# Performance work log

Measured on AMD Instinct MI355X. Metric: run time of the kernel, lower is better.

Reference implementation:

```python
import jax, jax.numpy as jnp
import numpy as np
from jax.scipy.special import logsumexp

B, T = 32, 512
WV, CV = 32000, 8000
DW, DC = 128, 64
H = 128          # hidden per direction (hidden_size // 2)
L = 32           # num_labels


def setup_inputs() -> dict:
    key = jax.random.key(0)
    ks = jax.random.split(key, 16)
    D = DW + DC
    def n(k, shape, s=0.1):
        return jax.random.normal(k, shape, jnp.float32) * s
    return {
        'word': jax.random.randint(ks[0], (B, T), 1, WV),
        'char': jax.random.randint(ks[1], (B, T), 1, CV),  # >0 so mask is all ones
        'y': jax.random.randint(ks[2], (B, T), 0, L),
        'wordemb': n(ks[3], (WV, DW)),
        'charemb': n(ks[4], (CV, DC)),
        'W_ih_f': n(ks[5], (4 * H, D)), 'W_hh_f': n(ks[6], (4 * H, H)), 'b_f': n(ks[7], (4 * H,)),
        'W_ih_b': n(ks[8], (4 * H, D)), 'W_hh_b': n(ks[9], (4 * H, H)), 'b_b': n(ks[10], (4 * H,)),
        'W_out': n(ks[11], (L, 2 * H)), 'b_out': n(ks[12], (L,)),
        'trans': n(ks[13], (L, L)), 'start': n(ks[14], (L,)), 'end': n(ks[15], (L,)),
    }


def _lstm_scan(x_proj, W_hh):
    # x_proj: [T, B, 4H] = x @ W_ih.T + b, precomputed (batched GEMM)
    h0 = jnp.zeros((x_proj.shape[1], W_hh.shape[1]), x_proj.dtype)
    def step(carry, xt):
        h, c = carry
        g = xt + h @ W_hh.T                      # [B, 4H]
        i, f, gg, o = jnp.split(g, 4, axis=-1)   # PyTorch gate order i,f,g,o
        c = jax.nn.sigmoid(f) * c + jax.nn.sigmoid(i) * jnp.tanh(gg)
        h = jax.nn.sigmoid(o) * jnp.tanh(c)
        return (h, c), h
    _, hs = jax.lax.scan(step, (h0, h0), x_proj)
    return hs  # [T, B, H]


def reference(word, char, y, wordemb, charemb, W_ih_f, W_hh_f, b_f,
              W_ih_b, W_hh_b, b_b, W_out, b_out, trans, start, end):
    mask = (char > 0).astype(jnp.float32)                 # [B, T]
    x = jnp.concatenate([wordemb[word], charemb[char]], axis=-1)  # [B, T, D]

    # BiLSTM
    xp_f = (jnp.einsum('btd,gd->tbg', x, W_ih_f) + b_f)   # [T, B, 4H]
    xp_b = (jnp.einsum('btd,gd->tbg', x, W_ih_b) + b_b)[::-1]
    h_f = _lstm_scan(xp_f, W_hh_f)                        # [T, B, H]
    h_b = _lstm_scan(xp_b, W_hh_b)[::-1]                  # [T, B, H]
    h = jnp.concatenate([h_f, h_b], axis=-1).transpose(1, 0, 2)  # [B, T, 2H]

    emit = (jnp.einsum('bth,lh->btl', h, W_out) + b_out) * mask[:, :, None]  # [B, T, L]

    # CRF log-partition (forward algorithm)
    alpha0 = start + emit[:, 0]                           # [B, L]
    def crf_step(alpha, inp):
        e_t, m_t = inp                                    # [B, L], [B]
        new = logsumexp(alpha[:, :, None] + trans, axis=1) + e_t
        alpha = jnp.where(m_t[:, None] > 0, new, alpha)
        return alpha, None
    alpha, _ = jax.lax.scan(crf_step, alpha0,
                            (emit.transpose(1, 0, 2)[1:], mask.T[1:]))
    logZ = logsumexp(alpha + end, axis=-1)                # [B]

    # gold path score
    emit_score = (jnp.take_along_axis(emit, y[:, :, None], axis=-1)[..., 0] * mask).sum(1)
    trans_score = (trans[y[:, :-1], y[:, 1:]] * mask[:, 1:]).sum(1)
    last = mask.sum(1).astype(jnp.int32) - 1
    y_last = y[jnp.arange(y.shape[0]), last]
    gold = start[y[:, 0]] + emit_score + trans_score + end[y_last]

    return jnp.sum(logZ - gold)  # NLL, summed over batch
```

## Files before the change

kernel.cpp:

```cpp
#include <hip/hip_runtime.h>
#include <math.h>

#define BB 32
#define TT 512
#define DW 128
#define DC 64
#define DD 192
#define HH 128
#define G4 512
#define LL 32

typedef __fp16 h2_t __attribute__((ext_vector_type(2)));

__device__ __forceinline__ float qxor1(float x) {
    return __int_as_float(__builtin_amdgcn_update_dpp(0, __float_as_int(x), 0xB1, 0xF, 0xF, true));
}
__device__ __forceinline__ float qxor2(float x) {
    return __int_as_float(__builtin_amdgcn_update_dpp(0, __float_as_int(x), 0x4E, 0xF, 0xF, true));
}
__device__ __forceinline__ float qbcast(float x, int ctrl_imm) {
    switch (ctrl_imm) {
        case 0: return __int_as_float(__builtin_amdgcn_update_dpp(0, __float_as_int(x), 0x00, 0xF, 0xF, true));
        case 1: return __int_as_float(__builtin_amdgcn_update_dpp(0, __float_as_int(x), 0x55, 0xF, 0xF, true));
        case 2: return __int_as_float(__builtin_amdgcn_update_dpp(0, __float_as_int(x), 0xAA, 0xF, 0xF, true));
        default:return __int_as_float(__builtin_amdgcn_update_dpp(0, __float_as_int(x), 0xFF, 0xF, 0xF, true));
    }
}

__global__ __launch_bounds__(256) void k_inproj(
    const int* __restrict__ word, const int* __restrict__ charr,
    const float* __restrict__ wemb, const float* __restrict__ cemb,
    const float* __restrict__ Wf, const float* __restrict__ bf,
    const float* __restrict__ Wb, const float* __restrict__ bb,
    float* __restrict__ xpf, float* __restrict__ xpb)
{
    __shared__ __align__(16) h2_t As2[4][132];
    __shared__ __align__(16) h2_t Bs2[4][132];
    const int tid = threadIdx.x;
    const int ntile = blockIdx.x;
    const int ctile = blockIdx.y;
    const int dir = ctile >> 2;
    const float* W = dir ? Wb : Wf;
    const float* bias = dir ? bb : bf;
    float* xp = dir ? xpb : xpf;
    const int colbase = (ctile & 3) * 128;

    const int tr = tid >> 4;
    const int tc = tid & 15;

    float acc[8][8];
#pragma unroll
    for (int i = 0; i < 8; ++i)
#pragma unroll
        for (int j = 0; j < 8; ++j) acc[i][j] = 0.f;

    const int lrow = tid >> 1;
    const int lk   = (tid & 1) * 4;
    const int kp0  = lk >> 1;
    const int nA   = ntile * 128 + lrow;
    const int wi   = word[nA];
    const int ci   = charr[nA];
    const int g    = colbase + lrow;

    for (int kc = 0; kc < 24; ++kc) {
        const int k0 = kc * 8 + lk;
        float4 av;
        if (k0 < DW) av = *(const float4*)(wemb + (size_t)wi * DW + k0);
        else         av = *(const float4*)(cemb + (size_t)ci * DC + (k0 - DW));
        const float4 bv = *(const float4*)(W + (size_t)g * DD + k0);
        __syncthreads();
        As2[kp0 + 0][lrow] = __builtin_amdgcn_cvt_pkrtz(av.x, av.y);
        As2[kp0 + 1][lrow] = __builtin_amdgcn_cvt_pkrtz(av.z, av.w);
        Bs2[kp0 + 0][lrow] = __builtin_amdgcn_cvt_pkrtz(bv.x, bv.y);
        Bs2[kp0 + 1][lrow] = __builtin_amdgcn_cvt_pkrtz(bv.z, bv.w);
        __syncthreads();
#pragma unroll
        for (int kp = 0; kp < 4; ++kp) {
            h2_t __attribute__((aligned(16))) a2[8], b2[8];
            *(uint4*)&a2[0] = *(const uint4*)&As2[kp][tr * 8];
            *(uint4*)&a2[4] = *(const uint4*)&As2[kp][tr * 8 + 4];
            *(uint4*)&b2[0] = *(const uint4*)&Bs2[kp][tc * 8];
            *(uint4*)&b2[4] = *(const uint4*)&Bs2[kp][tc * 8 + 4];
#pragma unroll
            for (int i = 0; i < 8; ++i)
#pragma unroll
                for (int j = 0; j < 8; ++j)
                    acc[i][j] = __builtin_amdgcn_fdot2(a2[i], b2[j], acc[i][j], false);
        }
    }
#pragma unroll
    for (int i = 0; i < 8; ++i) {
        const int n  = ntile * 128 + tr * 8 + i;
        const int b_ = n >> 9, t_ = n & 511;
        float* dst = xp + ((size_t)(t_ * BB + b_)) * G4 + colbase + tc * 8;
#pragma unroll
        for (int j = 0; j < 8; ++j) dst[j] = acc[i][j] + bias[colbase + tc * 8 + j];
    }
}

__global__ __launch_bounds__(512)
__attribute__((amdgpu_waves_per_eu(2, 2)))
void k_lstm(
    const float* __restrict__ xpf, const float* __restrict__ xpb,
    const float* __restrict__ Whf, const float* __restrict__ Whb,
    float* __restrict__ hf, float* __restrict__ hb)
{
    __shared__ __align__(16) __fp16 hsd[2][160];
    const int tid = threadIdx.x;
    const int dir = blockIdx.x >> 5;
    const int b_  = blockIdx.x & 31;
    const float* xp = dir ? xpb : xpf;
    const float* Wh = dir ? Whb : Whf;
    float* hout = dir ? hb : hf;
    const int ks = tid & 3;
    const int u  = tid >> 2;

    h2_t w2[4][16];
#pragma unroll
    for (int g = 0; g < 4; ++g) {
        const float2* wp = (const float2*)(Wh + (size_t)(g * 128 + u) * HH + ks * 32);
#pragma unroll
        for (int j = 0; j < 16; ++j)
            w2[g][j] = __builtin_amdgcn_cvt_pkrtz(wp[j].x, wp[j].y);
    }

    const float mk0 = (ks == 0) ? 1.f : 0.f;
    const float mk1 = (ks == 1) ? 1.f : 0.f;
    const float mk2 = (ks == 2) ? 1.f : 0.f;
    const float mk3 = (ks == 3) ? 1.f : 0.f;
    const bool istanh = (ks == 2);
    const float GS  = istanh ? 2.f : -1.f;
    const float GC0 = istanh ? 1.f : 0.f;
    const float GC1 = istanh ? -2.f : 1.f;
    const bool ks1 = (ks & 1) != 0;
    const bool ks2 = (ks & 2) != 0;

    if (tid < 80) ((unsigned int*)&hsd[0][0])[tid] = 0u;
    float c = 0.f;
    const int t0 = dir ? (TT - 1) : 0;
    const int tstep = dir ? -1 : 1;
    const int xstride = tstep * BB * G4;
    const int hstride = tstep * BB * HH;
    const float* xqp = xp + ((long long)t0 * BB + b_) * G4 + ks * 128 + u;
    float*       hop = hout + ((long long)t0 * BB + b_) * HH + u;
    float xq = *xqp;
    __syncthreads();

    for (int s = 0; s < TT; ++s) {
        const int rb = s & 1;
        float p0 = mk0 * xq, p1 = mk1 * xq, p2 = mk2 * xq, p3 = mk3 * xq;
        xqp += xstride;
        xq = *xqp;
#pragma unroll
        for (int q = 0; q < 4; ++q) {
            const uint4 hv = *(const uint4*)&hsd[rb][ks * 40 + q * 8];
            const h2_t ha  = __builtin_bit_cast(h2_t, hv.x);
            const h2_t hbv = __builtin_bit_cast(h2_t, hv.y);
            const h2_t hc  = __builtin_bit_cast(h2_t, hv.z);
            const h2_t hd  = __builtin_bit_cast(h2_t, hv.w);
            p0 = __builtin_amdgcn_fdot2(ha,  w2[0][q*4+0], p0, false);
            p0 = __builtin_amdgcn_fdot2(hbv, w2[0][q*4+1], p0, false);
            p0 = __builtin_amdgcn_fdot2(hc,  w2[0][q*4+2], p0, false);
            p0 = __builtin_amdgcn_fdot2(hd,  w2[0][q*4+3], p0, false);
            p1 = __builtin_amdgcn_fdot2(ha,  w2[1][q*4+0], p1, false);
            p1 = __builtin_amdgcn_fdot2(hbv, w2[1][q*4+1], p1, false);
            p1 = __builtin_amdgcn_fdot2(hc,  w2[1][q*4+2], p1, false);
            p1 = __builtin_amdgcn_fdot2(hd,  w2[1][q*4+3], p1, false);
            p2 = __builtin_amdgcn_fdot2(ha,  w2[2][q*4+0], p2, false);
            p2 = __builtin_amdgcn_fdot2(hbv, w2[2][q*4+1], p2, false);
            p2 = __builtin_amdgcn_fdot2(hc,  w2[2][q*4+2], p2, false);
            p2 = __builtin_amdgcn_fdot2(hd,  w2[2][q*4+3], p2, false);
            p3 = __builtin_amdgcn_fdot2(ha,  w2[3][q*4+0], p3, false);
            p3 = __builtin_amdgcn_fdot2(hbv, w2[3][q*4+1], p3, false);
            p3 = __builtin_amdgcn_fdot2(hc,  w2[3][q*4+2], p3, false);
            p3 = __builtin_amdgcn_fdot2(hd,  w2[3][q*4+3], p3, false);
        }
        p0 += qxor1(p0); p0 += qxor2(p0);
        p1 += qxor1(p1); p1 += qxor2(p1);
        p2 += qxor1(p2); p2 += qxor2(p2);
        p3 += qxor1(p3); p3 += qxor2(p3);
        const float pa   = ks1 ? p1 : p0;
        const float pb   = ks1 ? p3 : p2;
        const float psel = ks2 ? pb : pa;
        const float val  = GC0 + GC1 * __builtin_amdgcn_rcpf(1.f + __expf(GS * psel));
        const float gi = qbcast(val, 0);
        const float gf = qbcast(val, 1);
        const float gg = qbcast(val, 2);
        const float go = qbcast(val, 3);
        c = gf * c + gi * gg;
        const float tc = 1.f - 2.f * __builtin_amdgcn_rcpf(1.f + __expf(2.f * c));
        const float hv = go * tc;
        if (ks == 0) {
            hsd[rb ^ 1][(u >> 5) * 40 + (u & 31)] = (__fp16)hv;
            *hop = hv;
        }
        hop += hstride;
        __builtin_amdgcn_sched_barrier(0);
        asm volatile("s_waitcnt lgkmcnt(0)");
        __builtin_amdgcn_s_barrier();
        __builtin_amdgcn_sched_barrier(0);
    }
}

__global__ __launch_bounds__(1024) void k_emit(
    const float* __restrict__ hf, const float* __restrict__ hb,
    const float* __restrict__ Wout, const float* __restrict__ bout,
    const int* __restrict__ charr, float* __restrict__ emit)
{
    __shared__ __align__(16) float hsm[BB * 256];
    __shared__ __align__(16) float wsm[LL * 260];
    const int t = blockIdx.x;
    const int tid = threadIdx.x;
    for (int idx = tid; idx < BB * 256; idx += 1024) {
        const int b_ = idx >> 8, u = idx & 255;
        hsm[idx] = (u < HH) ? hf[((size_t)t * BB + b_) * HH + u]
                            : hb[((size_t)t * BB + b_) * HH + (u - HH)];
    }
    for (int idx = tid; idx < LL * 256; idx += 1024) {
        const int l = idx >> 8, u = idx & 255;
        wsm[l * 260 + u] = Wout[idx];
    }
    __syncthreads();
    const int b_ = tid >> 5, l = tid & 31;
    float acc = bout[l];
#pragma unroll 8
    for (int q = 0; q < 64; ++q) {
        const float4 h4 = *(const float4*)&hsm[b_ * 256 + q * 4];
        const float4 w4 = *(const float4*)&wsm[l * 260 + q * 4];
        acc += h4.x * w4.x + h4.y * w4.y + h4.z * w4.z + h4.w * w4.w;
    }
    const float m = (charr[b_ * TT + t] > 0) ? 1.f : 0.f;
    emit[((size_t)t * BB + b_) * LL + l] = acc * m;
}

__global__ __launch_bounds__(64) void k_crf(
    const float* __restrict__ emit, const int* __restrict__ charr,
    const float* __restrict__ trans, const float* __restrict__ startv,
    const float* __restrict__ endv, float* __restrict__ logZ)
{
    const int tid = threadIdx.x;
    const int b_ = blockIdx.x;
    const int j = tid & 31;
    float et[32];
#pragma unroll
    for (int i = 0; i < 32; ++i) et[i] = __expf(trans[i * LL + j]);

    const float a0 = startv[j] + emit[(size_t)b_ * LL + j];
    float M = a0;
    M = fmaxf(M, __shfl_xor(M, 16));
    M = fmaxf(M, __shfl_xor(M, 8));
    M = fmaxf(M, __shfl_xor(M, 4));
    M = fmaxf(M, __shfl_xor(M, 2));
    M = fmaxf(M, __shfl_xor(M, 1));
    float A = __expf(a0 - M);
    float logsc = M;

    float e_nx = emit[((size_t)1 * BB + b_) * LL + j];
    int   m_nx = charr[b_ * TT + 1];

    for (int t = 1; t < TT; ++t) {
        const float ee = __expf(e_nx);
        const int m_cur = m_nx;
        if (t + 1 < TT) {
            e_nx = emit[((size_t)(t + 1) * BB + b_) * LL + j];
            m_nx = charr[b_ * TT + t + 1];
        }
        float s0 = 0.f, s1 = 0.f, s2 = 0.f, s3 = 0.f;
#pragma unroll
        for (int i = 0; i < 32; i += 4) {
            s0 = fmaf(__shfl(A, i    ), et[i    ], s0);
            s1 = fmaf(__shfl(A, i + 1), et[i + 1], s1);
            s2 = fmaf(__shfl(A, i + 2), et[i + 2], s2);
            s3 = fmaf(__shfl(A, i + 3), et[i + 3], s3);
        }
        const float Anew = ((s0 + s1) + (s2 + s3)) * ee;
        A = (m_cur > 0) ? Anew : A;
        if ((t & 7) == 0) {
            float S = A;
            S = fmaxf(S, __shfl_xor(S, 16));
            S = fmaxf(S, __shfl_xor(S, 8));
            S = fmaxf(S, __shfl_xor(S, 4));
            S = fmaxf(S, __shfl_xor(S, 2));
            S = fmaxf(S, __shfl_xor(S, 1));
            A *= __builtin_amdgcn_rcpf(S);
            logsc += __logf(S);
        }
    }
    const float z = __logf(A) + logsc + endv[j];
    float Mz = z;
    Mz = fmaxf(Mz, __shfl_xor(Mz, 16));
    Mz = fmaxf(Mz, __shfl_xor(Mz, 8));
    Mz = fmaxf(Mz, __shfl_xor(Mz, 4));
    Mz = fmaxf(Mz, __shfl_xor(Mz, 2));
    Mz = fmaxf(Mz, __shfl_xor(Mz, 1));
    float sz = __expf(z - Mz);
    sz += __shfl_xor(sz, 16);
    sz += __shfl_xor(sz, 8);
    sz += __shfl_xor(sz, 4);
    sz += __shfl_xor(sz, 2);
    sz += __shfl_xor(sz, 1);
    if (tid == 0) logZ[b_] = Mz + __logf(sz);
}

__global__ __launch_bounds__(1024) void k_gold(
    const float* __restrict__ emit, const int* __restrict__ charr,
    const int* __restrict__ y, const float* __restrict__ trans,
    const float* __restrict__ startv, const float* __restrict__ endv,
    const float* __restrict__ logZ, float* __restrict__ out)
{
    __shared__ float red[BB];
    const int tid = threadIdx.x;
    const int b_ = tid >> 5, l = tid & 31;
    float sc = 0.f;
    int ms = 0;
    for (int t = l; t < TT; t += 32) {
        const int yv = y[b_ * TT + t];
        const int m = (charr[b_ * TT + t] > 0);
        if (m) { sc += emit[((size_t)t * BB + b_) * LL + yv]; ms++; }
        if (t + 1 < TT) {
            const int mn = (charr[b_ * TT + t + 1] > 0);
            if (mn) sc += trans[yv * LL + y[b_ * TT + t + 1]];
        }
    }
#pragma unroll
    for (int o = 16; o; o >>= 1) {
        sc += __shfl_xor(sc, o);
        ms += __shfl_xor(ms, o);
    }
    if (l == 0) {
        int last = ms - 1;
        if (last < 0) last = 0;
        const float gold = startv[y[b_ * TT]] + sc + endv[y[b_ * TT + last]];
        red[b_] = logZ[b_] - gold;
    }
    __syncthreads();
    if (tid == 0) {
        float tot = 0.f;
#pragma unroll
        for (int i = 0; i < BB; ++i) tot += red[i];
        out[0] = tot;
    }
}

extern "C" void kernel_launch(void* const* d_in, const int* in_sizes, int n_in,
                              void* d_out, int out_size, void* d_ws, size_t ws_size,
                              hipStream_t stream) {
    (void)in_sizes; (void)n_in; (void)out_size; (void)ws_size;
    const int*   word  = (const int*)d_in[0];
    const int*   charr = (const int*)d_in[1];
    const int*   yv    = (const int*)d_in[2];
    const float* wemb  = (const float*)d_in[3];
    const float* cemb  = (const float*)d_in[4];
    const float* Wihf  = (const float*)d_in[5];
    const float* Whhf  = (const float*)d_in[6];
    const float* bf    = (const float*)d_in[7];
    const float* Wihb  = (const float*)d_in[8];
    const float* Whhb  = (const float*)d_in[9];
    const float* bb    = (const float*)d_in[10];
    const float* Wout  = (const float*)d_in[11];
    const float* bout  = (const float*)d_in[12];
    const float* trans = (const float*)d_in[13];
    const float* startv= (const float*)d_in[14];
    const float* endv  = (const float*)d_in[15];

    float* ws   = (float*)d_ws;
    float* xpf  = ws;
    float* xpb  = xpf + (size_t)TT * BB * G4;
    float* hf   = xpb + (size_t)TT * BB * G4;
    float* hb   = hf + (size_t)TT * BB * HH;
    float* emit = hb + (size_t)TT * BB * HH;
    float* logZ = emit + (size_t)TT * BB * LL;

    k_inproj<<<dim3(128, 8), 256, 0, stream>>>(word, charr, wemb, cemb,
                                               Wihf, bf, Wihb, bb, xpf, xpb);
    k_lstm<<<64, 512, 0, stream>>>(xpf, xpb, Whhf, Whhb, hf, hb);
    k_emit<<<TT, 1024, 0, stream>>>(hf, hb, Wout, bout, charr, emit);
    k_crf<<<32, 64, 0, stream>>>(emit, charr, trans, startv, endv, logZ);
    k_gold<<<1, 1024, 0, stream>>>(emit, charr, yv, trans, startv, endv, logZ,
                                   (float*)d_out);
}
```

Before: 537.1 us.

## Process two batch rows per LSTM block and prefetch inproj loads

The LSTM recurrence kernel now handles two batch sequences per workgroup (32 blocks instead of 64). The register-resident W_hh weights are reused for both sequences, which doubles the independent dot-product chains per step and hides latency in the serial step loop. The input-projection GEMM also software-prefetches the next k-chunk's global loads before the compute of the current chunk. The cost is twice the per-step work in each block and fewer active CUs, so the critical path per timestep may lengthen.

```diff
diff --git a/kernel.cpp b/kernel.cpp
--- a/kernel.cpp
+++ b/kernel.cpp
@@ -12,6 +12,8 @@
 
 typedef __fp16 h2_t __attribute__((ext_vector_type(2)));
 
+__device__ __forceinline__ h2_t bch2(unsigned int x) { return __builtin_bit_cast(h2_t, x); }
+
 __device__ __forceinline__ float qxor1(float x) {
     return __int_as_float(__builtin_amdgcn_update_dpp(0, __float_as_int(x), 0xB1, 0xF, 0xF, true));
 }
@@ -62,18 +64,22 @@
     const int ci   = charr[nA];
     const int g    = colbase + lrow;
 
+    float4 av = *(const float4*)(wemb + (size_t)wi * DW + lk);
+    float4 bv = *(const float4*)(W + (size_t)g * DD + lk);
+
     for (int kc = 0; kc < 24; ++kc) {
-        const int k0 = kc * 8 + lk;
-        float4 av;
-        if (k0 < DW) av = *(const float4*)(wemb + (size_t)wi * DW + k0);
-        else         av = *(const float4*)(cemb + (size_t)ci * DC + (k0 - DW));
-        const float4 bv = *(const float4*)(W + (size_t)g * DD + k0);
         __syncthreads();
         As2[kp0 + 0][lrow] = __builtin_amdgcn_cvt_pkrtz(av.x, av.y);
         As2[kp0 + 1][lrow] = __builtin_amdgcn_cvt_pkrtz(av.z, av.w);
         Bs2[kp0 + 0][lrow] = __builtin_amdgcn_cvt_pkrtz(bv.x, bv.y);
         Bs2[kp0 + 1][lrow] = __builtin_amdgcn_cvt_pkrtz(bv.z, bv.w);
         __syncthreads();
+        const int kcn = (kc + 1 < 24) ? (kc + 1) : 23;
+        const int k0n = kcn * 8 + lk;
+        float4 avn, bvn;
+        if (k0n < DW) avn = *(const float4*)(wemb + (size_t)wi * DW + k0n);
+        else          avn = *(const float4*)(cemb + (size_t)ci * DC + (k0n - DW));
+        bvn = *(const float4*)(W + (size_t)g * DD + k0n);
 #pragma unroll
         for (int kp = 0; kp < 4; ++kp) {
             h2_t __attribute__((aligned(16))) a2[8], b2[8];
@@ -87,6 +93,7 @@
                 for (int j = 0; j < 8; ++j)
                     acc[i][j] = __builtin_amdgcn_fdot2(a2[i], b2[j], acc[i][j], false);
         }
+        av = avn; bv = bvn;
     }
 #pragma unroll
     for (int i = 0; i < 8; ++i) {
@@ -105,10 +112,10 @@
     const float* __restrict__ Whf, const float* __restrict__ Whb,
     float* __restrict__ hf, float* __restrict__ hb)
 {
-    __shared__ __align__(16) __fp16 hsd[2][160];
-    const int tid = threadIdx.x;
-    const int dir = blockIdx.x >> 5;
-    const int b_  = blockIdx.x & 31;
+    __shared__ __align__(16) __fp16 hsd[2][2][160];
+    const int tid = threadIdx.x;
+    const int dir = blockIdx.x >> 4;
+    const int b0  = (blockIdx.x & 15) * 2;
     const float* xp = dir ? xpb : xpf;
     const float* Wh = dir ? Whb : Whf;
     float* hout = dir ? hb : hf;
@@ -133,66 +140,77 @@
     const float GC0 = istanh ? 1.f : 0.f;
     const float GC1 = istanh ? -2.f : 1.f;
     const bool ks1 = (ks & 1) != 0;
-    const bool ks2 = (ks & 2) != 0;
-
-    if (tid < 80) ((unsigned int*)&hsd[0][0])[tid] = 0u;
-    float c = 0.f;
+    const bool ks2b = (ks & 2) != 0;
+
+    if (tid < 160) ((unsigned int*)&hsd[0][0][0])[tid] = 0u;
+    float c0 = 0.f, c1 = 0.f;
     const int t0 = dir ? (TT - 1) : 0;
     const int tstep = dir ? -1 : 1;
     const int xstride = tstep * BB * G4;
     const int hstride = tstep * BB * HH;
-    const float* xqp = xp + ((long long)t0 * BB + b_) * G4 + ks * 128 + u;
-    float*       hop = hout + ((long long)t0 * BB + b_) * HH + u;
-    float xq = *xqp;
+    const float* xqp = xp + ((long long)t0 * BB + b0) * G4 + ks * 128 + u;
+    float*       hop = hout + ((long long)t0 * BB + b0) * HH + u;
+    float xq0 = xqp[0], xq1 = xqp[G4];
     __syncthreads();
 
     for (int s = 0; s < TT; ++s) {
         const int rb = s & 1;
-        float p0 = mk0 * xq, p1 = mk1 * xq, p2 = mk2 * xq, p3 = mk3 * xq;
+        float pA0 = mk0 * xq0, pA1 = mk1 * xq0, pA2 = mk2 * xq0, pA3 = mk3 * xq0;
+        float pB0 = mk0 * xq1, pB1 = mk1 * xq1, pB2 = mk2 * xq1, pB3 = mk3 * xq1;
         xqp += xstride;
-        xq = *xqp;
+        xq0 = xqp[0]; xq1 = xqp[G4];
 #pragma unroll
         for (int q = 0; q < 4; ++q) {
-            const uint4 hv = *(const uint4*)&hsd[rb][ks * 40 + q * 8];
-            const h2_t ha  = __builtin_bit_cast(h2_t, hv.x);
-            const h2_t hbv = __builtin_bit_cast(h2_t, hv.y);
-            const h2_t hc  = __builtin_bit_cast(h2_t, hv.z);
-            const h2_t hd  = __builtin_bit_cast(h2_t, hv.w);
-            p0 = __builtin_amdgcn_fdot2(ha,  w2[0][q*4+0], p0, false);
-            p0 = __builtin_amdgcn_fdot2(hbv, w2[0][q*4+1], p0, false);
-            p0 = __builtin_amdgcn_fdot2(hc,  w2[0][q*4+2], p0, false);
-            p0 = __builtin_amdgcn_fdot2(hd,  w2[0][q*4+3], p0, false);
-            p1 = __builtin_amdgcn_fdot2(ha,  w2[1][q*4+0], p1, false);
-            p1 = __builtin_amdgcn_fdot2(hbv, w2[1][q*4+1], p1, false);
-            p1 = __builtin_amdgcn_fdot2(hc,  w2[1][q*4+2], p1, false);
-            p1 = __builtin_amdgcn_fdot2(hd,  w2[1][q*4+3], p1, false);
-            p2 = __builtin_amdgcn_fdot2(ha,  w2[2][q*4+0], p2, false);
-            p2 = __builtin_amdgcn_fdot2(hbv, w2[2][q*4+1], p2, false);
-            p2 = __builtin_amdgcn_fdot2(hc,  w2[2][q*4+2], p2, false);
-            p2 = __builtin_amdgcn_fdot2(hd,  w2[2][q*4+3], p2, false);
-            p3 = __builtin_amdgcn_fdot2(ha,  w2[3][q*4+0], p3, false);
-            p3 = __builtin_amdgcn_fdot2(hbv, w2[3][q*4+1], p3, false);
-            p3 = __builtin_amdgcn_fdot2(hc,  w2[3][q*4+2], p3, false);
-            p3 = __builtin_amdgcn_fdot2(hd,  w2[3][q*4+3], p3, false);
-        }
-        p0 += qxor1(p0); p0 += qxor2(p0);
-        p1 += qxor1(p1); p1 += qxor2(p1);
-        p2 += qxor1(p2); p2 += qxor2(p2);
-        p3 += qxor1(p3); p3 += qxor2(p3);
-        const float pa   = ks1 ? p1 : p0;
-        const float pb   = ks1 ? p3 : p2;
-        const float psel = ks2 ? pb : pa;
-        const float val  = GC0 + GC1 * __builtin_amdgcn_rcpf(1.f + __expf(GS * psel));
-        const float gi = qbcast(val, 0);
-        const float gf = qbcast(val, 1);
-        const float gg = qbcast(val, 2);
-        const float go = qbcast(val, 3);
-        c = gf * c + gi * gg;
-        const float tc = 1.f - 2.f * __builtin_amdgcn_rcpf(1.f + __expf(2.f * c));
-        const float hv = go * tc;
+            const uint4 hva = *(const uint4*)&hsd[rb][0][ks * 40 + q * 8];
+            const uint4 hvb = *(const uint4*)&hsd[rb][1][ks * 40 + q * 8];
+            h2_t ha[4], hbv[4];
+            ha[0] = bch2(hva.x); ha[1] = bch2(hva.y); ha[2] = bch2(hva.z); ha[3] = bch2(hva.w);
+            hbv[0] = bch2(hvb.x); hbv[1] = bch2(hvb.y); hbv[2] = bch2(hvb.z); hbv[3] = bch2(hvb.w);
+#pragma unroll
+            for (int e = 0; e < 4; ++e) {
+                const h2_t ae = ha[e];
+                const h2_t be = hbv[e];
+                pA0 = __builtin_amdgcn_fdot2(ae, w2[0][q*4+e], pA0, false);
+                pB0 = __builtin_amdgcn_fdot2(be, w2[0][q*4+e], pB0, false);
+                pA1 = __builtin_amdgcn_fdot2(ae, w2[1][q*4+e], pA1, false);
+                pB1 = __builtin_amdgcn_fdot2(be, w2[1][q*4+e], pB1, false);
+                pA2 = __builtin_amdgcn_fdot2(ae, w2[2][q*4+e], pA2, false);
+                pB2 = __builtin_amdgcn_fdot2(be, w2[2][q*4+e], pB2, false);
+                pA3 = __builtin_amdgcn_fdot2(ae, w2[3][q*4+e], pA3, false);
+                pB3 = __builtin_amdgcn_fdot2(be, w2[3][q*4+e], pB3, false);
+            }
+        }
+        pA0 += qxor1(pA0); pB0 += qxor1(pB0);
+        pA1 += qxor1(pA1); pB1 += qxor1(pB1);
+        pA2 += qxor1(pA2); pB2 += qxor1(pB2);
+        pA3 += qxor1(pA3); pB3 += qxor1(pB3);
+        pA0 += qxor2(pA0); pB0 += qxor2(pB0);
+        pA1 += qxor2(pA1); pB1 += qxor2(pB1);
+        pA2 += qxor2(pA2); pB2 += qxor2(pB2);
+        pA3 += qxor2(pA3); pB3 += qxor2(pB3);
+        const float pa0 = ks1 ? pA1 : pA0;
+        const float pb0 = ks1 ? pA3 : pA2;
+        const float psel0 = ks2b ? pb0 : pa0;
+        const float pa1 = ks1 ? pB1 : pB0;
+        const float pb1 = ks1 ? pB3 : pB2;
+        const float psel1 = ks2b ? pb1 : pa1;
+        const float val0 = GC0 + GC1 * __builtin_amdgcn_rcpf(1.f + __expf(GS * psel0));
+        const float val1 = GC0 + GC1 * __builtin_amdgcn_rcpf(1.f + __expf(GS * psel1));
+        const float gi0 = qbcast(val0, 0), gi1 = qbcast(val1, 0);
+        const float gf0 = qbcast(val0, 1), gf1 = qbcast(val1, 1);
+        const float gg0 = qbcast(val0, 2), gg1 = qbcast(val1, 2);
+        const float go0 = qbcast(val0, 3), go1 = qbcast(val1, 3);
+        c0 = gf0 * c0 + gi0 * gg0;
+        c1 = gf1 * c1 + gi1 * gg1;
+        const float tc0 = 1.f - 2.f * __builtin_amdgcn_rcpf(1.f + __expf(2.f * c0));
+        const float tc1 = 1.f - 2.f * __builtin_amdgcn_rcpf(1.f + __expf(2.f * c1));
+        const float hv0 = go0 * tc0;
+        const float hv1 = go1 * tc1;
         if (ks == 0) {
-            hsd[rb ^ 1][(u >> 5) * 40 + (u & 31)] = (__fp16)hv;
-            *hop = hv;
+            hsd[rb ^ 1][0][(u >> 5) * 40 + (u & 31)] = (__fp16)hv0;
+            hsd[rb ^ 1][1][(u >> 5) * 40 + (u & 31)] = (__fp16)hv1;
+            hop[0]  = hv0;
+            hop[HH] = hv1;
         }
         hop += hstride;
         __builtin_amdgcn_sched_barrier(0);
@@ -373,7 +391,7 @@
 
     k_inproj<<<dim3(128, 8), 256, 0, stream>>>(word, charr, wemb, cemb,
                                                Wihf, bf, Wihb, bb, xpf, xpb);
-    k_lstm<<<64, 512, 0, stream>>>(xpf, xpb, Whhf, Whhb, hf, hb);
+    k_lstm<<<32, 512, 0, stream>>>(xpf, xpb, Whhf, Whhb, hf, hb);
     k_emit<<<TT, 1024, 0, stream>>>(hf, hb, Wout, bout, charr, emit);
     k_crf<<<32, 64, 0, stream>>>(emit, charr, trans, startv, endv, logZ);
     k_gold<<<1, 1024, 0, stream>>>(emit, charr, yv, trans, startv, endv, logZ,
```

Result: slower. 725.3 us (+35.0%).

## Stage full K in LDS for input projection and use readlane in CRF

Applied to the files above, without the earlier changes.

The input-projection GEMM now loads the entire K=192 slice of both A (gathered embeddings) and B (weights) into LDS once. It uses a wider 128x256 tile with 512 threads, replacing the per-chunk double-sync loop, which cuts barrier count and raises reuse. The CRF recurrence swaps __shfl for readlane scalar broadcasts, avoiding LDS-permute shuffles on the serial critical path. The larger LDS footprint (~150KB) may reduce occupancy to one block per CU.

```diff
diff --git a/kernel.cpp b/kernel.cpp
--- a/kernel.cpp
+++ b/kernel.cpp
@@ -12,6 +12,8 @@
 
 typedef __fp16 h2_t __attribute__((ext_vector_type(2)));
 
+__device__ __forceinline__ h2_t bch2(unsigned int x) { return __builtin_bit_cast(h2_t, x); }
+
 __device__ __forceinline__ float qxor1(float x) {
     return __int_as_float(__builtin_amdgcn_update_dpp(0, __float_as_int(x), 0xB1, 0xF, 0xF, true));
 }
@@ -27,55 +29,68 @@
     }
 }
 
-__global__ __launch_bounds__(256) void k_inproj(
+__global__ __launch_bounds__(512) void k_inproj(
     const int* __restrict__ word, const int* __restrict__ charr,
     const float* __restrict__ wemb, const float* __restrict__ cemb,
     const float* __restrict__ Wf, const float* __restrict__ bf,
     const float* __restrict__ Wb, const float* __restrict__ bb,
     float* __restrict__ xpf, float* __restrict__ xpb)
 {
-    __shared__ __align__(16) h2_t As2[4][132];
-    __shared__ __align__(16) h2_t Bs2[4][132];
+    __shared__ __align__(16) h2_t As2[96][132];
+    __shared__ __align__(16) h2_t Bs2[96][260];
     const int tid = threadIdx.x;
     const int ntile = blockIdx.x;
     const int ctile = blockIdx.y;
-    const int dir = ctile >> 2;
+    const int dir = ctile >> 1;
     const float* W = dir ? Wb : Wf;
     const float* bias = dir ? bb : bf;
     float* xp = dir ? xpb : xpf;
-    const int colbase = (ctile & 3) * 128;
-
-    const int tr = tid >> 4;
-    const int tc = tid & 15;
-
+    const int colbase = (ctile & 1) * 256;
+
+    {
+        const int lrow = tid >> 2;
+        const int lq   = tid & 3;
+        const int nA   = ntile * 128 + lrow;
+        const int wi   = word[nA];
+        const int ci   = charr[nA];
+#pragma unroll
+        for (int kc = 0; kc < 12; ++kc) {
+            const int k0 = kc * 16 + lq * 4;
+            float4 av;
+            if (k0 < DW) av = *(const float4*)(wemb + (size_t)wi * DW + k0);
+            else         av = *(const float4*)(cemb + (size_t)ci * DC + (k0 - DW));
+            const int kp = k0 >> 1;
+            As2[kp    ][lrow] = __builtin_amdgcn_cvt_pkrtz(av.x, av.y);
+            As2[kp + 1][lrow] = __builtin_amdgcn_cvt_pkrtz(av.z, av.w);
+        }
+    }
+    {
+        const int lcol = tid >> 1;
+        const int lh   = tid & 1;
+        const int g    = colbase + lcol;
+#pragma unroll
+        for (int kc = 0; kc < 24; ++kc) {
+            const int k0 = kc * 8 + lh * 4;
+            const float4 bv = *(const float4*)(W + (size_t)g * DD + k0);
+            const int kp = k0 >> 1;
+            Bs2[kp    ][lcol] = __builtin_amdgcn_cvt_pkrtz(bv.x, bv.y);
+            Bs2[kp + 1][lcol] = __builtin_amdgcn_cvt_pkrtz(bv.z, bv.w);
+        }
+    }
+    __syncthreads();
+
+    const int tr = tid >> 5;
+    const int tc = tid & 31;
     float acc[8][8];
 #pragma unroll
     for (int i = 0; i < 8; ++i)
 #pragma unroll
         for (int j = 0; j < 8; ++j) acc[i][j] = 0.f;
 
-    const int lrow = tid >> 1;
-    const int lk   = (tid & 1) * 4;
-    const int kp0  = lk >> 1;
-    const int nA   = ntile * 128 + lrow;
-    const int wi   = word[nA];
-    const int ci   = charr[nA];
-    const int g    = colbase + lrow;
-
     for (int kc = 0; kc < 24; ++kc) {
-        const int k0 = kc * 8 + lk;
-        float4 av;
-        if (k0 < DW) av = *(const float4*)(wemb + (size_t)wi * DW + k0);
-        else         av = *(const float4*)(cemb + (size_t)ci * DC + (k0 - DW));
-        const float4 bv = *(const float4*)(W + (size_t)g * DD + k0);
-        __syncthreads();
-        As2[kp0 + 0][lrow] = __builtin_amdgcn_cvt_pkrtz(av.x, av.y);
-        As2[kp0 + 1][lrow] = __builtin_amdgcn_cvt_pkrtz(av.z, av.w);
-        Bs2[kp0 + 0][lrow] = __builtin_amdgcn_cvt_pkrtz(bv.x, bv.y);
-        Bs2[kp0 + 1][lrow] = __builtin_amdgcn_cvt_pkrtz(bv.z, bv.w);
-        __syncthreads();
-#pragma unroll
-        for (int kp = 0; kp < 4; ++kp) {
+#pragma unroll
+        for (int kq = 0; kq < 4; ++kq) {
+            const int kp = kc * 4 + kq;
             h2_t __attribute__((aligned(16))) a2[8], b2[8];
             *(uint4*)&a2[0] = *(const uint4*)&As2[kp][tr * 8];
             *(uint4*)&a2[4] = *(const uint4*)&As2[kp][tr * 8 + 4];
@@ -154,10 +169,10 @@
 #pragma unroll
         for (int q = 0; q < 4; ++q) {
             const uint4 hv = *(const uint4*)&hsd[rb][ks * 40 + q * 8];
-            const h2_t ha  = __builtin_bit_cast(h2_t, hv.x);
-            const h2_t hbv = __builtin_bit_cast(h2_t, hv.y);
-            const h2_t hc  = __builtin_bit_cast(h2_t, hv.z);
-            const h2_t hd  = __builtin_bit_cast(h2_t, hv.w);
+            const h2_t ha  = bch2(hv.x);
+            const h2_t hbv = bch2(hv.y);
+            const h2_t hc  = bch2(hv.z);
+            const h2_t hd  = bch2(hv.w);
             p0 = __builtin_amdgcn_fdot2(ha,  w2[0][q*4+0], p0, false);
             p0 = __builtin_amdgcn_fdot2(hbv, w2[0][q*4+1], p0, false);
             p0 = __builtin_amdgcn_fdot2(hc,  w2[0][q*4+2], p0, false);
@@ -268,10 +283,10 @@
         float s0 = 0.f, s1 = 0.f, s2 = 0.f, s3 = 0.f;
 #pragma unroll
         for (int i = 0; i < 32; i += 4) {
-            s0 = fmaf(__shfl(A, i    ), et[i    ], s0);
-            s1 = fmaf(__shfl(A, i + 1), et[i + 1], s1);
-            s2 = fmaf(__shfl(A, i + 2), et[i + 2], s2);
-            s3 = fmaf(__shfl(A, i + 3), et[i + 3], s3);
+            s0 = fmaf(__int_as_float(__builtin_amdgcn_readlane(__float_as_int(A), i    )), et[i    ], s0);
+            s1 = fmaf(__int_as_float(__builtin_amdgcn_readlane(__float_as_int(A), i + 1)), et[i + 1], s1);
+            s2 = fmaf(__int_as_float(__builtin_amdgcn_readlane(__float_as_int(A), i + 2)), et[i + 2], s2);
+            s3 = fmaf(__int_as_float(__builtin_amdgcn_readlane(__float_as_int(A), i + 3)), et[i + 3], s3);
         }
         const float Anew = ((s0 + s1) + (s2 + s3)) * ee;
         A = (m_cur > 0) ? Anew : A;
@@ -371,7 +386,7 @@
     float* emit = hb + (size_t)TT * BB * HH;
     float* logZ = emit + (size_t)TT * BB * LL;
 
-    k_inproj<<<dim3(128, 8), 256, 0, stream>>>(word, charr, wemb, cemb,
+    k_inproj<<<dim3(128, 4), 512, 0, stream>>>(word, charr, wemb, cemb,
                                                Wihf, bf, Wihb, bb, xpf, xpb);
     k_lstm<<<64, 512, 0, stream>>>(xpf, xpb, Whhf, Whhb, hf, hb);
     k_emit<<<TT, 1024, 0, stream>>>(hf, hb, Wout, bout, charr, emit);
```

New measurement: 507.6 us. 1.06x faster.
